# Kernel optimization log

Measured on AMD Instinct MI355X. Metric: run time of the kernel, lower is better.

The kernel has to match this reference:

```python
import jax, jax.numpy as jnp
import numpy as np

N_NODES = 100000
N_EDGES = 1600000
FEAT = 64
HIDDEN = 64
NUM_GRAPHS = 64


def gcn_conv(x, row, col, norm, W, b, n_nodes):
    # x: [N, in], W: [in, out]; PyG GCNConv: transform, then normalized scatter-add, then bias
    xw = x @ W                                   # [N, out]
    msgs = xw[row] * norm[:, None]               # [E+N, out]
    out = jax.ops.segment_sum(msgs, col, num_segments=n_nodes)
    return out + b


def _norm_and_loops(edge_index, n_nodes):
    # add self loops and compute symmetric normalization deg^-1/2 * deg^-1/2
    loop = jnp.arange(n_nodes, dtype=edge_index.dtype)
    row = jnp.concatenate([edge_index[0], loop])  # sources
    col = jnp.concatenate([edge_index[1], loop])  # targets
    ew = jnp.ones(row.shape[0], dtype=jnp.float32)
    deg = jax.ops.segment_sum(ew, col, num_segments=n_nodes)
    dinv = jnp.where(deg > 0, jax.lax.rsqrt(jnp.maximum(deg, 1.0)), 0.0)
    norm = dinv[row] * dinv[col]
    return row, col, norm


def setup_inputs() -> dict:
    key = jax.random.key(0)
    ks = jax.random.split(key, 10)
    x = jax.random.normal(ks[0], (N_NODES, FEAT), dtype=jnp.float32)
    edge_index = jax.random.randint(ks[1], (2, N_EDGES), 0, N_NODES, dtype=jnp.int64 if jax.config.jax_enable_x64 else jnp.int32)
    batch = jnp.sort(jax.random.randint(ks[2], (N_NODES,), 0, NUM_GRAPHS, dtype=edge_index.dtype))
    def xavier(k, fan_in, fan_out):
        lim = np.sqrt(6.0 / (fan_in + fan_out))
        return jax.random.uniform(k, (fan_in, fan_out), minval=-lim, maxval=lim, dtype=jnp.float32)
    W1 = xavier(ks[3], FEAT, HIDDEN)
    W2 = xavier(ks[4], HIDDEN, HIDDEN)
    W3 = xavier(ks[5], HIDDEN, HIDDEN)
    b1 = jnp.zeros((HIDDEN,), jnp.float32)
    b2 = jnp.zeros((HIDDEN,), jnp.float32)
    b3 = jnp.zeros((HIDDEN,), jnp.float32)
    return {"x": x, "edge_index": edge_index, "batch": batch,
            "W1": W1, "b1": b1, "W2": W2, "b2": b2, "W3": W3, "b3": b3}


def reference(x, edge_index, batch, W1, b1, W2, b2, W3, b3):
    n_nodes = x.shape[0]
    row, col, norm = _norm_and_loops(edge_index, n_nodes)
    xs = []
    h = x
    for W, b in ((W1, b1), (W2, b2), (W3, b3)):
        h = gcn_conv(h, row, col, norm, W, b, n_nodes)
        h = jax.nn.relu(h)
        xs.append(h)
    # global_add_pool per layer, then concat along features -> [num_graphs, 3*hidden]
    pooled = [jax.ops.segment_sum(h, batch, num_segments=NUM_GRAPHS) for h in xs]
    return jnp.concatenate(pooled, axis=1)
```

## Files before the change

kernel.cpp:

```cpp
#include <hip/hip_runtime.h>


#define F 64
#define CAP 48
#define NPW 16
#define NRANGE 8

typedef __attribute__((ext_vector_type(8))) short short8x;
typedef __attribute__((ext_vector_type(4))) float f32x4;

static inline size_t alignup(size_t x, size_t a) { return (x + a - 1) & ~(a - 1); }

__device__ __forceinline__ ushort f2bf(float f) {
    unsigned u = __builtin_bit_cast(unsigned, f);
    unsigned r = (u + 0x7fffu + ((u >> 16) & 1u)) >> 16;
    return (ushort)r;
}
__device__ __forceinline__ float bf2f(ushort v) {
    return __builtin_bit_cast(float, ((unsigned)v) << 16);
}
__device__ __forceinline__ float4 bf4_to_f4(ushort4 v) {
    return make_float4(bf2f(v.x), bf2f(v.y), bf2f(v.z), bf2f(v.w));
}

__global__ __launch_bounds__(256) void k_build(const int* __restrict__ rowv,
                                               const int* __restrict__ colv,
                                               int* __restrict__ cnt,
                                               int* __restrict__ csr,
                                               int E, int rsize) {
    int r = blockIdx.x & (NRANGE - 1);
    int e4 = (blockIdx.x >> 3) * 256 + threadIdx.x;
    int lo = r * rsize;
    int hiEx = lo + rsize;
    int E4 = E >> 2;
    if (e4 < E4) {
        int4 c = ((const int4*)colv)[e4];
        int4 s = ((const int4*)rowv)[e4];
        int p;
        if (c.x >= lo && c.x < hiEx) {
            p = atomicAdd(&cnt[c.x], 1);
            if (p < CAP) csr[(size_t)c.x * CAP + p] = s.x;
        }
        if (c.y >= lo && c.y < hiEx) {
            p = atomicAdd(&cnt[c.y], 1);
            if (p < CAP) csr[(size_t)c.y * CAP + p] = s.y;
        }
        if (c.z >= lo && c.z < hiEx) {
            p = atomicAdd(&cnt[c.z], 1);
            if (p < CAP) csr[(size_t)c.z * CAP + p] = s.z;
        }
        if (c.w >= lo && c.w < hiEx) {
            p = atomicAdd(&cnt[c.w], 1);
            if (p < CAP) csr[(size_t)c.w * CAP + p] = s.w;
        }
    }
    int tail = E & 3;
    if (r == 0 && (int)blockIdx.x < NRANGE && (int)threadIdx.x < tail) {
        int e = (E4 << 2) + threadIdx.x;
        int c = colv[e], s = rowv[e];
        int p = atomicAdd(&cnt[c], 1);
        if (p < CAP) csr[(size_t)c * CAP + p] = s;
    }
}

__global__ __launch_bounds__(256) void k_prepx(const float* __restrict__ x,
                                               ushort* __restrict__ xbf, long n4) {
    long i = (long)blockIdx.x * 256 + threadIdx.x;
    if (i < n4) {
        float4 v = ((const float4*)x)[i];
        ushort4 u;
        u.x = f2bf(v.x); u.y = f2bf(v.y); u.z = f2bf(v.z); u.w = f2bf(v.w);
        ((ushort4*)xbf)[i] = u;
    }
}

__global__ __launch_bounds__(256) void k_prepw(const float* __restrict__ W0,
                                               const float* __restrict__ W1,
                                               const float* __restrict__ W2,
                                               ushort* __restrict__ wt) {
    const float* W = (blockIdx.x == 0) ? W0 : (blockIdx.x == 1) ? W1 : W2;
    ushort* o = wt + (size_t)blockIdx.x * F * F;
    for (int i = threadIdx.x; i < F * F; i += 256) {
        int k = i >> 6, c = i & 63;
        o[c * F + k] = f2bf(W[i]);
    }
}

__global__ __launch_bounds__(256) void k_gemm(const ushort* __restrict__ Hbf,
                                              const ushort* __restrict__ WT,
                                              const int* __restrict__ cnt,
                                              ushort* __restrict__ XW, int n) {
    __shared__ ushort hl[64][72];
    __shared__ ushort wl[64][72];
    int rowBase = blockIdx.x * 64;
    for (int i = threadIdx.x; i < 1024; i += 256) {
        int idx = i & 511;
        int row = idx >> 3, cb = (idx & 7) << 3;
        if (i < 512) {
            int gr = rowBase + row;
            short8x v = {0, 0, 0, 0, 0, 0, 0, 0};
            if (gr < n) v = *(const short8x*)(Hbf + (size_t)gr * F + cb);
            *(short8x*)&hl[row][cb] = v;
        } else {
            *(short8x*)&wl[row][cb] = *(const short8x*)(WT + row * F + cb);
        }
    }
    __syncthreads();

    int lane = threadIdx.x & 63;
    int w = threadIdx.x >> 6;
    int l15 = lane & 15, l4 = lane >> 4;

    short8x a0 = *(const short8x*)&hl[w * 16 + l15][l4 * 8];
    short8x a1 = *(const short8x*)&hl[w * 16 + l15][32 + l4 * 8];

    f32x4 acc[4];
#pragma unroll
    for (int ct = 0; ct < 4; ++ct) {
        acc[ct] = (f32x4){0.f, 0.f, 0.f, 0.f};
        short8x b0 = *(const short8x*)&wl[ct * 16 + l15][l4 * 8];
        short8x b1 = *(const short8x*)&wl[ct * 16 + l15][32 + l4 * 8];
        acc[ct] = __builtin_amdgcn_mfma_f32_16x16x32_bf16(a0, b0, acc[ct], 0, 0, 0);
        acc[ct] = __builtin_amdgcn_mfma_f32_16x16x32_bf16(a1, b1, acc[ct], 0, 0, 0);
    }

#pragma unroll
    for (int r = 0; r < 4; ++r) {
        int gr = rowBase + w * 16 + l4 * 4 + r;
        if (gr < n) {
            float sc = rsqrtf((float)cnt[gr] + 1.0f);
#pragma unroll
            for (int ct = 0; ct < 4; ++ct) {
                XW[(size_t)gr * F + ct * 16 + l15] = f2bf(acc[ct][r] * sc);
            }
        }
    }
}

__global__ __launch_bounds__(256) void k_gather(const ushort* __restrict__ XW,
                                                const int* __restrict__ cnt,
                                                const int* __restrict__ csr,
                                                const float* __restrict__ bias,
                                                ushort* __restrict__ h,
                                                int n) {
    int lane = threadIdx.x & 63;
    int q = lane >> 4, s = lane & 15;
    int wave = blockIdx.x * (blockDim.x >> 6) + (threadIdx.x >> 6);
    int base = wave * NPW;
    if (base >= n) return;
    float4 bv = ((const float4*)bias)[s];
    const ushort4* XW4 = (const ushort4*)XW;
    for (int t = 0; t < NPW / 4; ++t) {
        int node = base + (t << 2) + q;
        if (node >= n) continue;
        int deg = cnt[node];
        const int* cr = csr + (size_t)node * CAP;
        float4 sum = bf4_to_f4(XW4[(size_t)node * 16 + s]);
        int j = 0;
        for (; j + 4 <= deg; j += 4) {
            int4 a = *(const int4*)(cr + j);
            float4 v0 = bf4_to_f4(XW4[(size_t)a.x * 16 + s]);
            float4 v1 = bf4_to_f4(XW4[(size_t)a.y * 16 + s]);
            float4 v2 = bf4_to_f4(XW4[(size_t)a.z * 16 + s]);
            float4 v3 = bf4_to_f4(XW4[(size_t)a.w * 16 + s]);
            sum.x += (v0.x + v1.x) + (v2.x + v3.x);
            sum.y += (v0.y + v1.y) + (v2.y + v3.y);
            sum.z += (v0.z + v1.z) + (v2.z + v3.z);
            sum.w += (v0.w + v1.w) + (v2.w + v3.w);
        }
        for (; j < deg; ++j) {
            float4 v = bf4_to_f4(XW4[(size_t)cr[j] * 16 + s]);
            sum.x += v.x; sum.y += v.y; sum.z += v.z; sum.w += v.w;
        }
        float sc = rsqrtf((float)deg + 1.0f);
        ushort4 hv;
        hv.x = f2bf(fmaxf(fmaf(sum.x, sc, bv.x), 0.f));
        hv.y = f2bf(fmaxf(fmaf(sum.y, sc, bv.y), 0.f));
        hv.z = f2bf(fmaxf(fmaf(sum.z, sc, bv.z), 0.f));
        hv.w = f2bf(fmaxf(fmaf(sum.w, sc, bv.w), 0.f));
        ((ushort4*)h)[(size_t)node * 16 + s] = hv;
    }
}

__global__ __launch_bounds__(256) void k_pool(const ushort* __restrict__ h,
                                              const int* __restrict__ batch,
                                              float* __restrict__ out,
                                              int layerOff, int n) {
    __shared__ int se[2];
    __shared__ float part[4][F];
    int g = blockIdx.x;
    if (threadIdx.x == 0) {
        int lo = 0, hi = n;
        while (lo < hi) { int mid = (lo + hi) >> 1; if (batch[mid] < g) lo = mid + 1; else hi = mid; }
        se[0] = lo;
        hi = n;
        while (lo < hi) { int mid = (lo + hi) >> 1; if (batch[mid] < g + 1) lo = mid + 1; else hi = mid; }
        se[1] = lo;
    }
    __syncthreads();
    int start = se[0], end = se[1];
    int f = threadIdx.x & 63;
    int w = threadIdx.x >> 6;
    float s0 = 0.f, s1 = 0.f, s2 = 0.f, s3 = 0.f;
    int node = start + w;
    for (; node + 12 < end; node += 16) {
        s0 += bf2f(h[(size_t)node * F + f]);
        s1 += bf2f(h[(size_t)(node + 4) * F + f]);
        s2 += bf2f(h[(size_t)(node + 8) * F + f]);
        s3 += bf2f(h[(size_t)(node + 12) * F + f]);
    }
    for (; node < end; node += 4) s0 += bf2f(h[(size_t)node * F + f]);
    part[w][f] = (s0 + s1) + (s2 + s3);
    __syncthreads();
    if (threadIdx.x < F) {
        float t = part[0][f] + part[1][f] + part[2][f] + part[3][f];
        out[g * (3 * F) + layerOff + f] = t;
    }
}

extern "C" void kernel_launch(void* const* d_in, const int* in_sizes, int n_in,
                              void* d_out, int out_size, void* d_ws, size_t ws_size,
                              hipStream_t stream) {
    const float* x = (const float*)d_in[0];
    const int* edge = (const int*)d_in[1];
    const int* batch = (const int*)d_in[2];
    const float* Ws[3] = {(const float*)d_in[3], (const float*)d_in[5], (const float*)d_in[7]};
    const float* bs[3] = {(const float*)d_in[4], (const float*)d_in[6], (const float*)d_in[8]};
    float* out = (float*)d_out;

    const int N = in_sizes[0] / F;
    const int E = in_sizes[1] / 2;
    const int* rowv = edge;
    const int* colv = edge + E;

    char* ws = (char*)d_ws;
    size_t off = 0;
    int*    cnt = (int*)(ws + off);    off = alignup(off + (size_t)N * 4, 256);
    int*    csr = (int*)(ws + off);    off = alignup(off + (size_t)N * CAP * 4, 256);
    ushort* xw  = (ushort*)(ws + off); off = alignup(off + (size_t)N * F * 2, 256);
    ushort* h   = (ushort*)(ws + off); off = alignup(off + (size_t)N * F * 2, 256);
    ushort* xbf = (ushort*)(ws + off); off = alignup(off + (size_t)N * F * 2, 256);
    ushort* wt  = (ushort*)(ws + off); off = alignup(off + (size_t)3 * F * F * 2, 256);
    (void)ws_size;

    hipMemsetAsync(cnt, 0, (size_t)N * 4, stream);

    const int rsize = (N + NRANGE - 1) / NRANGE;
    const int chunks = ((E >> 2) + 255) / 256;
    k_build<<<chunks * NRANGE, 256, 0, stream>>>(rowv, colv, cnt, csr, E, rsize);

    const long n4 = ((long)N * F) / 4;
    k_prepx<<<(int)((n4 + 255) / 256), 256, 0, stream>>>(x, xbf, n4);
    k_prepw<<<3, 256, 0, stream>>>(Ws[0], Ws[1], Ws[2], wt);

    const int gemmBlocks = (N + 63) / 64;
    const int gatherWaves = (N + NPW - 1) / NPW;
    const int gatherBlocks = (gatherWaves + 3) / 4;

    for (int l = 0; l < 3; ++l) {
        const ushort* Hin = (l == 0) ? xbf : h;
        k_gemm<<<gemmBlocks, 256, 0, stream>>>(Hin, wt + (size_t)l * F * F, cnt, xw, N);
        k_gather<<<gatherBlocks, 256, 0, stream>>>(xw, cnt, csr, bs[l], h, N);
        k_pool<<<64, 256, 0, stream>>>(h, batch, out, l * F, N);
    }
}
```

Baseline: 335.6 us.

## Split node features into 8-wide planes and gather per feature group

```diff
diff --git a/kernel.cpp b/kernel.cpp
--- a/kernel.cpp
+++ b/kernel.cpp
@@ -7,6 +7,7 @@
 #define NRANGE 8
 
 typedef __attribute__((ext_vector_type(8))) short short8x;
+typedef __attribute__((ext_vector_type(8))) unsigned short ushort8x;
 typedef __attribute__((ext_vector_type(4))) float f32x4;
 
 static inline size_t alignup(size_t x, size_t a) { return (x + a - 1) & ~(a - 1); }
@@ -18,9 +19,6 @@
 }
 __device__ __forceinline__ float bf2f(ushort v) {
     return __builtin_bit_cast(float, ((unsigned)v) << 16);
-}
-__device__ __forceinline__ float4 bf4_to_f4(ushort4 v) {
-    return make_float4(bf2f(v.x), bf2f(v.y), bf2f(v.z), bf2f(v.w));
 }
 
 __global__ __launch_bounds__(256) void k_build(const int* __restrict__ rowv,
@@ -64,14 +62,17 @@
 }
 
 __global__ __launch_bounds__(256) void k_prepx(const float* __restrict__ x,
-                                               ushort* __restrict__ xbf, long n4) {
+                                               ushort* __restrict__ xs,
+                                               int n, size_t nstride) {
     long i = (long)blockIdx.x * 256 + threadIdx.x;
-    if (i < n4) {
-        float4 v = ((const float4*)x)[i];
-        ushort4 u;
-        u.x = f2bf(v.x); u.y = f2bf(v.y); u.z = f2bf(v.z); u.w = f2bf(v.w);
-        ((ushort4*)xbf)[i] = u;
-    }
+    if (i >= (long)n * 8) return;
+    int node = (int)(i >> 3), fg = (int)(i & 7);
+    float4 a = ((const float4*)x)[(size_t)node * 16 + fg * 2];
+    float4 b = ((const float4*)x)[(size_t)node * 16 + fg * 2 + 1];
+    ushort8x o;
+    o[0] = f2bf(a.x); o[1] = f2bf(a.y); o[2] = f2bf(a.z); o[3] = f2bf(a.w);
+    o[4] = f2bf(b.x); o[5] = f2bf(b.y); o[6] = f2bf(b.z); o[7] = f2bf(b.w);
+    *(ushort8x*)(xs + (size_t)fg * nstride + (size_t)node * 8) = o;
 }
 
 __global__ __launch_bounds__(256) void k_prepw(const float* __restrict__ W0,
@@ -86,23 +87,25 @@
     }
 }
 
-__global__ __launch_bounds__(256) void k_gemm(const ushort* __restrict__ Hbf,
+__global__ __launch_bounds__(256) void k_gemm(const ushort* __restrict__ Hs,
                                               const ushort* __restrict__ WT,
                                               const int* __restrict__ cnt,
-                                              ushort* __restrict__ XW, int n) {
+                                              ushort* __restrict__ XWs,
+                                              int n, size_t nstride) {
     __shared__ ushort hl[64][72];
     __shared__ ushort wl[64][72];
     int rowBase = blockIdx.x * 64;
     for (int i = threadIdx.x; i < 1024; i += 256) {
-        int idx = i & 511;
-        int row = idx >> 3, cb = (idx & 7) << 3;
         if (i < 512) {
+            int fg = i >> 6, row = i & 63;
             int gr = rowBase + row;
-            short8x v = {0, 0, 0, 0, 0, 0, 0, 0};
-            if (gr < n) v = *(const short8x*)(Hbf + (size_t)gr * F + cb);
-            *(short8x*)&hl[row][cb] = v;
+            ushort8x v = {0, 0, 0, 0, 0, 0, 0, 0};
+            if (gr < n) v = *(const ushort8x*)(Hs + (size_t)fg * nstride + (size_t)gr * 8);
+            *(ushort8x*)&hl[row][fg * 8] = v;
         } else {
-            *(short8x*)&wl[row][cb] = *(const short8x*)(WT + row * F + cb);
+            int idx = i & 511;
+            int row = idx >> 3, cb = (idx & 7) << 3;
+            *(ushort8x*)&wl[row][cb] = *(const ushort8x*)(WT + row * F + cb);
         }
     }
     __syncthreads();
@@ -131,61 +134,72 @@
             float sc = rsqrtf((float)cnt[gr] + 1.0f);
 #pragma unroll
             for (int ct = 0; ct < 4; ++ct) {
-                XW[(size_t)gr * F + ct * 16 + l15] = f2bf(acc[ct][r] * sc);
+                int c = ct * 16 + l15;
+                XWs[(size_t)(c >> 3) * nstride + (size_t)gr * 8 + (c & 7)] =
+                    f2bf(acc[ct][r] * sc);
             }
         }
     }
 }
 
-__global__ __launch_bounds__(256) void k_gather(const ushort* __restrict__ XW,
+__global__ __launch_bounds__(256) void k_gather(const ushort* __restrict__ XWs,
                                                 const int* __restrict__ cnt,
                                                 const int* __restrict__ csr,
                                                 const float* __restrict__ bias,
-                                                ushort* __restrict__ h,
-                                                int n) {
+                                                ushort* __restrict__ hs,
+                                                int n, size_t nstride) {
+    int fg = blockIdx.x & 7;
+    int chunk = blockIdx.x >> 3;
     int lane = threadIdx.x & 63;
+    int w = threadIdx.x >> 6;
     int q = lane >> 4, s = lane & 15;
-    int wave = blockIdx.x * (blockDim.x >> 6) + (threadIdx.x >> 6);
-    int base = wave * NPW;
-    if (base >= n) return;
-    float4 bv = ((const float4*)bias)[s];
-    const ushort4* XW4 = (const ushort4*)XW;
+    const ushort* plane = XWs + (size_t)fg * nstride;
+    ushort* hplane = hs + (size_t)fg * nstride;
+    float bv[8];
+#pragma unroll
+    for (int i = 0; i < 8; ++i) bv[i] = bias[fg * 8 + i];
+    int nodeBase = (chunk * 4 + w) * NPW;
     for (int t = 0; t < NPW / 4; ++t) {
-        int node = base + (t << 2) + q;
-        if (node >= n) continue;
-        int deg = cnt[node];
-        const int* cr = csr + (size_t)node * CAP;
-        float4 sum = bf4_to_f4(XW4[(size_t)node * 16 + s]);
-        int j = 0;
-        for (; j + 4 <= deg; j += 4) {
-            int4 a = *(const int4*)(cr + j);
-            float4 v0 = bf4_to_f4(XW4[(size_t)a.x * 16 + s]);
-            float4 v1 = bf4_to_f4(XW4[(size_t)a.y * 16 + s]);
-            float4 v2 = bf4_to_f4(XW4[(size_t)a.z * 16 + s]);
-            float4 v3 = bf4_to_f4(XW4[(size_t)a.w * 16 + s]);
-            sum.x += (v0.x + v1.x) + (v2.x + v3.x);
-            sum.y += (v0.y + v1.y) + (v2.y + v3.y);
-            sum.z += (v0.z + v1.z) + (v2.z + v3.z);
-            sum.w += (v0.w + v1.w) + (v2.w + v3.w);
-        }
-        for (; j < deg; ++j) {
-            float4 v = bf4_to_f4(XW4[(size_t)cr[j] * 16 + s]);
-            sum.x += v.x; sum.y += v.y; sum.z += v.z; sum.w += v.w;
-        }
-        float sc = rsqrtf((float)deg + 1.0f);
-        ushort4 hv;
-        hv.x = f2bf(fmaxf(fmaf(sum.x, sc, bv.x), 0.f));
-        hv.y = f2bf(fmaxf(fmaf(sum.y, sc, bv.y), 0.f));
-        hv.z = f2bf(fmaxf(fmaf(sum.z, sc, bv.z), 0.f));
-        hv.w = f2bf(fmaxf(fmaf(sum.w, sc, bv.w), 0.f));
-        ((ushort4*)h)[(size_t)node * 16 + s] = hv;
-    }
-}
-
-__global__ __launch_bounds__(256) void k_pool(const ushort* __restrict__ h,
+        int node = nodeBase + (t << 2) + q;
+        bool valid = node < n;
+        float sum[8] = {0.f, 0.f, 0.f, 0.f, 0.f, 0.f, 0.f, 0.f};
+        int deg = 0, dmax = 0;
+        const int* cr = csr + (size_t)(valid ? node : 0) * CAP;
+        if (valid) {
+            deg = cnt[node];
+            dmax = min(deg, CAP);
+            if (s == 0) {
+                ushort8x v = *(const ushort8x*)(plane + (size_t)node * 8);
+#pragma unroll
+                for (int i = 0; i < 8; ++i) sum[i] += bf2f(v[i]);
+            }
+            for (int j = s; j < dmax; j += 16) {
+                int src = cr[j];
+                ushort8x v = *(const ushort8x*)(plane + (size_t)src * 8);
+#pragma unroll
+                for (int i = 0; i < 8; ++i) sum[i] += bf2f(v[i]);
+            }
+        }
+#pragma unroll
+        for (int m = 8; m >= 1; m >>= 1) {
+#pragma unroll
+            for (int i = 0; i < 8; ++i) sum[i] += __shfl_xor(sum[i], m, 64);
+        }
+        if (valid && s == 0) {
+            float sc = rsqrtf((float)deg + 1.0f);
+            ushort8x o;
+#pragma unroll
+            for (int i = 0; i < 8; ++i)
+                o[i] = f2bf(fmaxf(fmaf(sum[i], sc, bv[i]), 0.f));
+            *(ushort8x*)(hplane + (size_t)node * 8) = o;
+        }
+    }
+}
+
+__global__ __launch_bounds__(256) void k_pool(const ushort* __restrict__ hs,
                                               const int* __restrict__ batch,
                                               float* __restrict__ out,
-                                              int layerOff, int n) {
+                                              int layerOff, int n, size_t nstride) {
     __shared__ int se[2];
     __shared__ float part[4][F];
     int g = blockIdx.x;
@@ -201,15 +215,16 @@
     int start = se[0], end = se[1];
     int f = threadIdx.x & 63;
     int w = threadIdx.x >> 6;
+    const ushort* plane = hs + (size_t)(f >> 3) * nstride + (f & 7);
     float s0 = 0.f, s1 = 0.f, s2 = 0.f, s3 = 0.f;
     int node = start + w;
     for (; node + 12 < end; node += 16) {
-        s0 += bf2f(h[(size_t)node * F + f]);
-        s1 += bf2f(h[(size_t)(node + 4) * F + f]);
-        s2 += bf2f(h[(size_t)(node + 8) * F + f]);
-        s3 += bf2f(h[(size_t)(node + 12) * F + f]);
-    }
-    for (; node < end; node += 4) s0 += bf2f(h[(size_t)node * F + f]);
+        s0 += bf2f(plane[(size_t)node * 8]);
+        s1 += bf2f(plane[(size_t)(node + 4) * 8]);
+        s2 += bf2f(plane[(size_t)(node + 8) * 8]);
+        s3 += bf2f(plane[(size_t)(node + 12) * 8]);
+    }
+    for (; node < end; node += 4) s0 += bf2f(plane[(size_t)node * 8]);
     part[w][f] = (s0 + s1) + (s2 + s3);
     __syncthreads();
     if (threadIdx.x < F) {
@@ -232,6 +247,7 @@
     const int E = in_sizes[1] / 2;
     const int* rowv = edge;
     const int* colv = edge + E;
+    const size_t nstride = (size_t)N * 8;
 
     char* ws = (char*)d_ws;
     size_t off = 0;
@@ -249,18 +265,16 @@
     const int chunks = ((E >> 2) + 255) / 256;
     k_build<<<chunks * NRANGE, 256, 0, stream>>>(rowv, colv, cnt, csr, E, rsize);
 
-    const long n4 = ((long)N * F) / 4;
-    k_prepx<<<(int)((n4 + 255) / 256), 256, 0, stream>>>(x, xbf, n4);
+    k_prepx<<<(int)(((long)N * 8 + 255) / 256), 256, 0, stream>>>(x, xbf, N, nstride);
     k_prepw<<<3, 256, 0, stream>>>(Ws[0], Ws[1], Ws[2], wt);
 
     const int gemmBlocks = (N + 63) / 64;
-    const int gatherWaves = (N + NPW - 1) / NPW;
-    const int gatherBlocks = (gatherWaves + 3) / 4;
+    const int gchunks = (N + 4 * NPW - 1) / (4 * NPW);
 
     for (int l = 0; l < 3; ++l) {
         const ushort* Hin = (l == 0) ? xbf : h;
-        k_gemm<<<gemmBlocks, 256, 0, stream>>>(Hin, wt + (size_t)l * F * F, cnt, xw, N);
-        k_gather<<<gatherBlocks, 256, 0, stream>>>(xw, cnt, csr, bs[l], h, N);
-        k_pool<<<64, 256, 0, stream>>>(h, batch, out, l * F, N);
-    }
-}
+        k_gemm<<<gemmBlocks, 256, 0, stream>>>(Hin, wt + (size_t)l * F * F, cnt, xw, N, nstride);
+        k_gather<<<gchunks * 8, 256, 0, stream>>>(xw, cnt, csr, bs[l], h, N, nstride);
+        k_pool<<<64, 256, 0, stream>>>(h, batch, out, l * F, N, nstride);
+    }
+}
```

Measured after the change: 489.3 us. 1.46x slower.
